# Kernel tuning notes

Hardware: AMD Instinct MI355X
Metric: run time of the kernel (lower is better)

## Reference

```python
import jax, jax.numpy as jnp
import numpy as np

DIM = 256
WINDOW = 8
HEADS = 8
N = WINDOW * WINDOW


def _make_rpb_index(window_size: int) -> jnp.ndarray:
    hs = np.arange(window_size)
    coords = np.stack(np.meshgrid(hs, hs, indexing='ij'))  # [2, w, w]
    flat = coords.reshape(2, -1)                            # [2, N]
    rel = flat[:, :, None] - flat[:, None, :]               # [2, N, N]
    rel = rel.transpose(1, 2, 0).copy()                     # [N, N, 2]
    rel[:, :, 0] += window_size - 1
    rel[:, :, 1] += window_size - 1
    rel[:, :, 0] *= 2 * window_size - 1
    return jnp.asarray(rel.sum(-1), dtype=jnp.int32)        # [N, N]


def setup_inputs() -> dict:
    key = jax.random.key(0)
    k_x, k_qw, k_qb, k_pw, k_pb, k_rpb = jax.random.split(key, 6)
    B_ = 2048
    x = jax.random.normal(k_x, (B_, N, DIM), dtype=jnp.float32)
    mask = jnp.zeros((64, N, N), dtype=jnp.float32)
    # nn.Linear weights stored [out, in] as in torch
    qkv_w = jax.random.normal(k_qw, (3 * DIM, DIM), dtype=jnp.float32) * 0.02
    qkv_b = jnp.zeros((3 * DIM,), dtype=jnp.float32)
    proj_w = jax.random.normal(k_pw, (DIM, DIM), dtype=jnp.float32) * 0.02
    proj_b = jnp.zeros((DIM,), dtype=jnp.float32)
    rpb_table = jax.random.normal(k_rpb, ((2 * WINDOW - 1) ** 2, HEADS), dtype=jnp.float32) * 0.02
    rpb_index = _make_rpb_index(WINDOW)
    return {"x": x, "mask": mask, "qkv_w": qkv_w, "qkv_b": qkv_b,
            "proj_w": proj_w, "proj_b": proj_b, "rpb_table": rpb_table,
            "rpb_index": rpb_index}


def reference(x, mask, qkv_w, qkv_b, proj_w, proj_b, rpb_table, rpb_index):
    B_, n, C = x.shape
    H = HEADS
    d = C // H
    scale = d ** -0.5
    qkv = x @ qkv_w.T + qkv_b                      # [B, N, 3C]
    qkv = qkv.reshape(B_, n, 3, H, d)
    q = qkv[:, :, 0].transpose(0, 2, 1, 3)          # [B, H, N, d]
    k = qkv[:, :, 1].transpose(0, 2, 1, 3)
    v = qkv[:, :, 2].transpose(0, 2, 1, 3)
    attn = jnp.einsum('bhnd,bhmd->bhnm', q * scale, k)
    rpb = rpb_table[rpb_index]                      # [N, N, H]
    attn = attn + rpb.transpose(2, 0, 1)[None]      # [B, H, N, N]
    nW = mask.shape[0]
    attn = attn.reshape(B_ // nW, nW, H, n, n) + mask[None, :, None]
    attn = attn.reshape(B_, H, n, n)
    attn = jax.nn.softmax(attn, axis=-1)
    out = jnp.einsum('bhnm,bhmd->bhnd', attn, v)    # [B, H, N, d]
    out = out.transpose(0, 2, 1, 3).reshape(B_, n, C)
    return out @ proj_w.T + proj_b
```

## Files before the change

kernel.cpp:

```cpp
#include <hip/hip_runtime.h>
#include <hip/hip_bf16.h>


#define TOK 64
#define CDIM 256

typedef __attribute__((ext_vector_type(8))) short short8;
typedef __attribute__((ext_vector_type(4))) float f32x4;
typedef __attribute__((ext_vector_type(4))) float float4_t;

__device__ __forceinline__ short f2bf(float f) {
  union { float f; unsigned u; } v; v.f = f;
  unsigned r = v.u + 0x7FFFu + ((v.u >> 16) & 1u);
  return (short)(r >> 16);
}

__device__ __forceinline__ int rm_addr(int base, int row, int col) {
  return base + row * 512 + ((col * 2) ^ ((row & 7) << 4));
}

__global__ void preconv_kernel(const float* __restrict__ qkv_w,
                               const float* __restrict__ proj_w,
                               const float* __restrict__ rpb_table,
                               const int* __restrict__ rpb_index,
                               short* __restrict__ wqkv,
                               short* __restrict__ wproj,
                               float* __restrict__ rpb_pre) {
  int idx = blockIdx.x * blockDim.x + threadIdx.x;
  const float scale = 0.17677669529663687f;
  if (idx < 768 * 256) {
    float v = qkv_w[idx];
    if (idx < 256 * 256) v *= scale;
    wqkv[idx] = f2bf(v);
  } else if (idx < 768 * 256 + 256 * 256) {
    int i = idx - 768 * 256;
    wproj[i] = f2bf(proj_w[i]);
  } else if (idx < 768 * 256 + 256 * 256 + 8 * 64 * 64) {
    int i = idx - (768 * 256 + 256 * 256);
    int h = i >> 12;
    int nm = i & 4095;
    rpb_pre[i] = rpb_table[rpb_index[nm] * 8 + h];
  }
}

__global__ void __launch_bounds__(512, 2) fused_attn(
    const float* __restrict__ x, const float* __restrict__ mask,
    const float* __restrict__ qkv_b, const float* __restrict__ proj_b,
    const short* __restrict__ wqkv, const short* __restrict__ wproj,
    const float* __restrict__ rpb, float* __restrict__ out) {
  extern __shared__ char smem[];
  const int b = blockIdx.x;
  const int tid = threadIdx.x;
  const int w = tid >> 6;
  const int lane = tid & 63;
  const int lg = lane >> 4;
  const int ll = lane & 15;
  const float scale = 0.17677669529663687f;

  {
    const int row = tid >> 3;
    const int c0 = (tid & 7) * 32;
    const float4_t* src = reinterpret_cast<const float4_t*>(
        x + (size_t)b * TOK * CDIM + row * CDIM + c0);
    for (int j = 0; j < 4; ++j) {
      float4_t f0 = src[2 * j];
      float4_t f1 = src[2 * j + 1];
      short8 s;
      s[0] = f2bf(f0[0]); s[1] = f2bf(f0[1]); s[2] = f2bf(f0[2]); s[3] = f2bf(f0[3]);
      s[4] = f2bf(f1[0]); s[5] = f2bf(f1[1]); s[6] = f2bf(f1[2]); s[7] = f2bf(f1[3]);
      *reinterpret_cast<short8*>(smem + rm_addr(0, row, c0 + 8 * j)) = s;
    }
  }
  __syncthreads();

  f32x4 acc[4][6] = {};
  for (int ks = 0; ks < 8; ++ks) {
    int k0 = ks * 32;
    short8 a[4];
    for (int mi = 0; mi < 4; ++mi)
      a[mi] = *reinterpret_cast<const short8*>(
          smem + rm_addr(0, ll + 16 * mi, k0 + lg * 8));
    for (int j = 0; j < 6; ++j) {
      int s = j >> 1, hf = j & 1;
      int c = s * 256 + w * 32 + hf * 16 + ll;
      short8 bb = *reinterpret_cast<const short8*>(wqkv + c * 256 + k0 + lg * 8);
      for (int mi = 0; mi < 4; ++mi)
        acc[mi][j] = __builtin_amdgcn_mfma_f32_16x16x32_bf16(a[mi], bb, acc[mi][j], 0, 0, 0);
    }
  }
  for (int j = 0; j < 6; ++j) {
    int s = j >> 1, hf = j & 1;
    int c = s * 256 + w * 32 + hf * 16 + ll;
    float bias = qkv_b[c];
    if (s == 0) bias *= scale;
    for (int mi = 0; mi < 4; ++mi) {
      for (int r = 0; r < 4; ++r) {
        int row = lg * 4 + r + 16 * mi;
        short bf = f2bf(acc[mi][j][r] + bias);
        if (s == 0) {
          *reinterpret_cast<short*>(smem + rm_addr(32768, row, w * 32 + hf * 16 + ll)) = bf;
        } else if (s == 1) {
          *reinterpret_cast<short*>(smem + rm_addr(65536, row, w * 32 + hf * 16 + ll)) = bf;
        } else {
          int d = hf * 16 + ll;
          int addr = 98304 + w * 4096 + d * 128 + ((row * 2) ^ ((d & 7) << 4));
          *reinterpret_cast<short*>(smem + addr) = bf;
        }
      }
    }
  }
  __syncthreads();

  f32x4 sa[4][4];
  {
    short8 aq[4], bk[4];
    for (int mi = 0; mi < 4; ++mi)
      aq[mi] = *reinterpret_cast<const short8*>(
          smem + rm_addr(32768, ll + 16 * mi, w * 32 + lg * 8));
    for (int ni = 0; ni < 4; ++ni)
      bk[ni] = *reinterpret_cast<const short8*>(
          smem + rm_addr(65536, ll + 16 * ni, w * 32 + lg * 8));
    f32x4 z{0.0f, 0.0f, 0.0f, 0.0f};
    for (int mi = 0; mi < 4; ++mi)
      for (int ni = 0; ni < 4; ++ni)
        sa[mi][ni] = __builtin_amdgcn_mfma_f32_16x16x32_bf16(aq[mi], bk[ni], z, 0, 0, 0);
    const float* rp = rpb + w * 4096;
    const float* mk = mask + (size_t)(b & 63) * 4096;
    for (int mi = 0; mi < 4; ++mi)
      for (int r = 0; r < 4; ++r) {
        int row = lg * 4 + r + 16 * mi;
        for (int ni = 0; ni < 4; ++ni) {
          int col = ll + 16 * ni;
          sa[mi][ni][r] += rp[row * 64 + col] + mk[row * 64 + col];
        }
      }
  }

  float rinv[4][4];
  for (int mi = 0; mi < 4; ++mi)
    for (int r = 0; r < 4; ++r) {
      float m = sa[mi][0][r];
      for (int ni = 1; ni < 4; ++ni) m = fmaxf(m, sa[mi][ni][r]);
      for (int d = 1; d < 16; d <<= 1) m = fmaxf(m, __shfl_xor(m, d));
      float sum = 0.f;
      for (int ni = 0; ni < 4; ++ni) {
        float e = __expf(sa[mi][ni][r] - m);
        sa[mi][ni][r] = e;
        sum += e;
      }
      for (int d = 1; d < 16; d <<= 1) sum += __shfl_xor(sum, d);
      rinv[mi][r] = 1.0f / sum;
    }

  __syncthreads();

  {
    int base = w * 8192;
    for (int mi = 0; mi < 4; ++mi)
      for (int ni = 0; ni < 4; ++ni)
        for (int r = 0; r < 4; ++r) {
          int row = lg * 4 + r + 16 * mi;
          int col = ll + 16 * ni;
          int addr = base + row * 128 + ((col * 2) ^ ((row & 7) << 4));
          *reinterpret_cast<short*>(smem + addr) = f2bf(sa[mi][ni][r]);
        }
  }
  __syncthreads();

  f32x4 oa[4][2] = {};
  {
    int base = w * 8192;
    for (int ks = 0; ks < 2; ++ks) {
      short8 ap[4];
      for (int mi = 0; mi < 4; ++mi) {
        int row = ll + 16 * mi;
        int addr = base + row * 128 + (((ks * 32 + lg * 8) * 2) ^ ((row & 7) << 4));
        ap[mi] = *reinterpret_cast<const short8*>(smem + addr);
      }
      for (int nj = 0; nj < 2; ++nj) {
        int d = ll + 16 * nj;
        int addr = 98304 + w * 4096 + d * 128 + (((ks * 32 + lg * 8) * 2) ^ ((d & 7) << 4));
        short8 bv = *reinterpret_cast<const short8*>(smem + addr);
        for (int mi = 0; mi < 4; ++mi)
          oa[mi][nj] = __builtin_amdgcn_mfma_f32_16x16x32_bf16(ap[mi], bv, oa[mi][nj], 0, 0, 0);
      }
    }
  }
  for (int mi = 0; mi < 4; ++mi)
    for (int nj = 0; nj < 2; ++nj)
      for (int r = 0; r < 4; ++r) {
        int row = lg * 4 + r + 16 * mi;
        float v = oa[mi][nj][r] * rinv[mi][r];
        *reinterpret_cast<short*>(smem + rm_addr(65536, row, w * 32 + nj * 16 + ll)) = f2bf(v);
      }
  __syncthreads();

  f32x4 pa[4][2] = {};
  for (int ks = 0; ks < 8; ++ks) {
    int k0 = ks * 32;
    short8 a[4];
    for (int mi = 0; mi < 4; ++mi)
      a[mi] = *reinterpret_cast<const short8*>(
          smem + rm_addr(65536, ll + 16 * mi, k0 + lg * 8));
    for (int nj = 0; nj < 2; ++nj) {
      int c = w * 32 + nj * 16 + ll;
      short8 bb = *reinterpret_cast<const short8*>(wproj + c * 256 + k0 + lg * 8);
      for (int mi = 0; mi < 4; ++mi)
        pa[mi][nj] = __builtin_amdgcn_mfma_f32_16x16x32_bf16(a[mi], bb, pa[mi][nj], 0, 0, 0);
    }
  }
  float* outp = out + (size_t)b * TOK * CDIM;
  for (int nj = 0; nj < 2; ++nj) {
    int c = w * 32 + nj * 16 + ll;
    float bias = proj_b[c];
    for (int mi = 0; mi < 4; ++mi)
      for (int r = 0; r < 4; ++r) {
        int row = lg * 4 + r + 16 * mi;
        outp[row * 256 + c] = pa[mi][nj][r] + bias;
      }
  }
}

extern "C" void kernel_launch(void* const* d_in, const int* in_sizes, int n_in,
                              void* d_out, int out_size, void* d_ws, size_t ws_size,
                              hipStream_t stream) {
  const float* x        = (const float*)d_in[0];
  const float* mask     = (const float*)d_in[1];
  const float* qkv_w    = (const float*)d_in[2];
  const float* qkv_b    = (const float*)d_in[3];
  const float* proj_w   = (const float*)d_in[4];
  const float* proj_b   = (const float*)d_in[5];
  const float* rpb_tab  = (const float*)d_in[6];
  const int*   rpb_idx  = (const int*)d_in[7];
  float* out = (float*)d_out;

  short* wqkv = (short*)d_ws;
  short* wproj = wqkv + 768 * 256;
  float* rpb_pre = (float*)(wproj + 256 * 256);

  int total = 768 * 256 + 256 * 256 + 8 * 64 * 64;
  preconv_kernel<<<(total + 255) / 256, 256, 0, stream>>>(
      qkv_w, proj_w, rpb_tab, rpb_idx, wqkv, wproj, rpb_pre);

  hipFuncSetAttribute((const void*)fused_attn,
                      hipFuncAttributeMaxDynamicSharedMemorySize, 131072);
  int B = in_sizes[0] / (TOK * CDIM);
  fused_attn<<<B, 512, 131072, stream>>>(x, mask, qkv_b, proj_b, wqkv, wproj,
                                         rpb_pre, out);
}
```

Before: 243.2 us.

## Halve LDS footprint with per-wave Q/K/V/P buffers and vectorized bias loads

Reworks the shared-memory plan so each wave keeps its Q, K, V and P tiles in its own 8 KB region, with the x tile reusing space. This cuts dynamic LDS from 128 KB to 64 KB, and launch bounds are raised to allow more resident blocks per CU. The relative-position bias and mask are pre-permuted in the prep kernel so each lane reads them as float4. The P tile is written and consumed in two halves without block-wide barriers. The risk is higher register pressure from the 4-blocks launch bound and the extra mask preprocessing pass.

```diff
diff --git a/kernel.cpp b/kernel.cpp
--- a/kernel.cpp
+++ b/kernel.cpp
@@ -4,6 +4,7 @@
 
 #define TOK 64
 #define CDIM 256
+#define XOFF 32768
 
 typedef __attribute__((ext_vector_type(8))) short short8;
 typedef __attribute__((ext_vector_type(4))) float f32x4;
@@ -23,31 +24,51 @@
                                const float* __restrict__ proj_w,
                                const float* __restrict__ rpb_table,
                                const int* __restrict__ rpb_index,
+                               const float* __restrict__ mask,
                                short* __restrict__ wqkv,
                                short* __restrict__ wproj,
-                               float* __restrict__ rpb_pre) {
+                               float* __restrict__ rpbT,
+                               float* __restrict__ maskT) {
   int idx = blockIdx.x * blockDim.x + threadIdx.x;
   const float scale = 0.17677669529663687f;
-  if (idx < 768 * 256) {
+  const int NW1 = 768 * 256;
+  const int NW2 = NW1 + 256 * 256;
+  const int NW3 = NW2 + 8 * 64 * 64;
+  const int NW4 = NW3 + 64 * 64 * 64;
+  if (idx < NW1) {
     float v = qkv_w[idx];
     if (idx < 256 * 256) v *= scale;
     wqkv[idx] = f2bf(v);
-  } else if (idx < 768 * 256 + 256 * 256) {
-    int i = idx - 768 * 256;
+  } else if (idx < NW2) {
+    int i = idx - NW1;
     wproj[i] = f2bf(proj_w[i]);
-  } else if (idx < 768 * 256 + 256 * 256 + 8 * 64 * 64) {
-    int i = idx - (768 * 256 + 256 * 256);
+  } else if (idx < NW3) {
+    int i = idx - NW2;
     int h = i >> 12;
-    int nm = i & 4095;
-    rpb_pre[i] = rpb_table[rpb_index[nm] * 8 + h];
-  }
-}
-
-__global__ void __launch_bounds__(512, 2) fused_attn(
-    const float* __restrict__ x, const float* __restrict__ mask,
-    const float* __restrict__ qkv_b, const float* __restrict__ proj_b,
+    int pos = i & 4095;
+    int qtok = pos >> 6;
+    int t = pos & 63;
+    int llv = t >> 2, ni = t & 3;
+    int kt = ni * 16 + llv;
+    rpbT[i] = rpb_table[rpb_index[qtok * 64 + kt] * 8 + h];
+  } else if (idx < NW4) {
+    int i = idx - NW3;
+    int win = i >> 12;
+    int pos = i & 4095;
+    int qtok = pos >> 6;
+    int t = pos & 63;
+    int llv = t >> 2, ni = t & 3;
+    int kt = ni * 16 + llv;
+    maskT[i] = mask[win * 4096 + qtok * 64 + kt];
+  }
+}
+
+__global__ void __launch_bounds__(512, 4) fused_attn(
+    const float* __restrict__ x, const float* __restrict__ qkv_b,
+    const float* __restrict__ proj_b,
     const short* __restrict__ wqkv, const short* __restrict__ wproj,
-    const float* __restrict__ rpb, float* __restrict__ out) {
+    const float* __restrict__ rpbT, const float* __restrict__ maskT,
+    float* __restrict__ out) {
   extern __shared__ char smem[];
   const int b = blockIdx.x;
   const int tid = threadIdx.x;
@@ -56,6 +77,7 @@
   const int lg = lane >> 4;
   const int ll = lane & 15;
   const float scale = 0.17677669529663687f;
+  const int S0 = w * 8192, S1 = S0 + 4096;
 
   {
     const int row = tid >> 3;
@@ -68,7 +90,7 @@
       short8 s;
       s[0] = f2bf(f0[0]); s[1] = f2bf(f0[1]); s[2] = f2bf(f0[2]); s[3] = f2bf(f0[3]);
       s[4] = f2bf(f1[0]); s[5] = f2bf(f1[1]); s[6] = f2bf(f1[2]); s[7] = f2bf(f1[3]);
-      *reinterpret_cast<short8*>(smem + rm_addr(0, row, c0 + 8 * j)) = s;
+      *reinterpret_cast<short8*>(smem + rm_addr(XOFF, row, c0 + 8 * j)) = s;
     }
   }
   __syncthreads();
@@ -79,7 +101,7 @@
     short8 a[4];
     for (int mi = 0; mi < 4; ++mi)
       a[mi] = *reinterpret_cast<const short8*>(
-          smem + rm_addr(0, ll + 16 * mi, k0 + lg * 8));
+          smem + rm_addr(XOFF, ll + 16 * mi, k0 + lg * 8));
     for (int j = 0; j < 6; ++j) {
       int s = j >> 1, hf = j & 1;
       int c = s * 256 + w * 32 + hf * 16 + ll;
@@ -88,51 +110,58 @@
         acc[mi][j] = __builtin_amdgcn_mfma_f32_16x16x32_bf16(a[mi], bb, acc[mi][j], 0, 0, 0);
     }
   }
-  for (int j = 0; j < 6; ++j) {
+  __syncthreads();
+
+  for (int j = 0; j < 4; ++j) {
     int s = j >> 1, hf = j & 1;
     int c = s * 256 + w * 32 + hf * 16 + ll;
     float bias = qkv_b[c];
     if (s == 0) bias *= scale;
-    for (int mi = 0; mi < 4; ++mi) {
-      for (int r = 0; r < 4; ++r) {
-        int row = lg * 4 + r + 16 * mi;
-        short bf = f2bf(acc[mi][j][r] + bias);
-        if (s == 0) {
-          *reinterpret_cast<short*>(smem + rm_addr(32768, row, w * 32 + hf * 16 + ll)) = bf;
-        } else if (s == 1) {
-          *reinterpret_cast<short*>(smem + rm_addr(65536, row, w * 32 + hf * 16 + ll)) = bf;
-        } else {
-          int d = hf * 16 + ll;
-          int addr = 98304 + w * 4096 + d * 128 + ((row * 2) ^ ((d & 7) << 4));
-          *reinterpret_cast<short*>(smem + addr) = bf;
-        }
-      }
-    }
-  }
-  __syncthreads();
+    int base = (s == 0) ? S0 : S1;
+    int dl2 = (hf * 16 + ll) * 2;
+    for (int mi = 0; mi < 4; ++mi)
+      for (int r = 0; r < 4; ++r) {
+        int tok = lg * 4 + r + 16 * mi;
+        *reinterpret_cast<short*>(smem + base + tok * 64 + (dl2 ^ ((tok & 3) << 4))) =
+            f2bf(acc[mi][j][r] + bias);
+      }
+  }
+  short8 aq[4], bk[4];
+  for (int mi = 0; mi < 4; ++mi)
+    aq[mi] = *reinterpret_cast<const short8*>(
+        smem + S0 + (ll + 16 * mi) * 64 + ((lg * 16) ^ (((ll + 16 * mi) & 3) << 4)));
+  for (int ni = 0; ni < 4; ++ni)
+    bk[ni] = *reinterpret_cast<const short8*>(
+        smem + S1 + (ll + 16 * ni) * 64 + ((lg * 16) ^ (((ll + 16 * ni) & 3) << 4)));
+
+  for (int hf = 0; hf < 2; ++hf) {
+    int c = 2 * 256 + w * 32 + hf * 16 + ll;
+    float bias = qkv_b[c];
+    int d = hf * 16 + ll;
+    for (int mi = 0; mi < 4; ++mi)
+      for (int rp = 0; rp < 2; ++rp) {
+        int tok0 = lg * 4 + rp * 2 + 16 * mi;
+        unsigned u = (unsigned)(unsigned short)f2bf(acc[mi][4 + hf][2 * rp] + bias)
+                   | ((unsigned)(unsigned short)f2bf(acc[mi][4 + hf][2 * rp + 1] + bias) << 16);
+        *reinterpret_cast<unsigned*>(smem + S0 + d * 128 + ((tok0 * 2) ^ ((d & 7) << 4))) = u;
+      }
+  }
 
   f32x4 sa[4][4];
   {
-    short8 aq[4], bk[4];
-    for (int mi = 0; mi < 4; ++mi)
-      aq[mi] = *reinterpret_cast<const short8*>(
-          smem + rm_addr(32768, ll + 16 * mi, w * 32 + lg * 8));
-    for (int ni = 0; ni < 4; ++ni)
-      bk[ni] = *reinterpret_cast<const short8*>(
-          smem + rm_addr(65536, ll + 16 * ni, w * 32 + lg * 8));
     f32x4 z{0.0f, 0.0f, 0.0f, 0.0f};
     for (int mi = 0; mi < 4; ++mi)
       for (int ni = 0; ni < 4; ++ni)
         sa[mi][ni] = __builtin_amdgcn_mfma_f32_16x16x32_bf16(aq[mi], bk[ni], z, 0, 0, 0);
-    const float* rp = rpb + w * 4096;
-    const float* mk = mask + (size_t)(b & 63) * 4096;
-    for (int mi = 0; mi < 4; ++mi)
-      for (int r = 0; r < 4; ++r) {
-        int row = lg * 4 + r + 16 * mi;
-        for (int ni = 0; ni < 4; ++ni) {
-          int col = ll + 16 * ni;
-          sa[mi][ni][r] += rp[row * 64 + col] + mk[row * 64 + col];
-        }
+    const float4_t* rpT4 = reinterpret_cast<const float4_t*>(rpbT) + w * 1024;
+    const float4_t* mkT4 = reinterpret_cast<const float4_t*>(maskT) + (b & 63) * 1024;
+    for (int mi = 0; mi < 4; ++mi)
+      for (int r = 0; r < 4; ++r) {
+        int qtok = lg * 4 + r + 16 * mi;
+        float4_t f = rpT4[qtok * 16 + ll];
+        float4_t g = mkT4[qtok * 16 + ll];
+        for (int ni = 0; ni < 4; ++ni)
+          sa[mi][ni][r] += f[ni] + g[ni];
       }
   }
 
@@ -152,46 +181,40 @@
       rinv[mi][r] = 1.0f / sum;
     }
 
-  __syncthreads();
-
-  {
-    int base = w * 8192;
-    for (int mi = 0; mi < 4; ++mi)
-      for (int ni = 0; ni < 4; ++ni)
+  f32x4 oa[4][2] = {};
+  for (int ks = 0; ks < 2; ++ks) {
+    for (int mi = 0; mi < 4; ++mi)
+      for (int nio = 0; nio < 2; ++nio) {
+        int ni = 2 * ks + nio;
+        int ktl2 = (nio * 16 + ll) * 2;
         for (int r = 0; r < 4; ++r) {
-          int row = lg * 4 + r + 16 * mi;
-          int col = ll + 16 * ni;
-          int addr = base + row * 128 + ((col * 2) ^ ((row & 7) << 4));
-          *reinterpret_cast<short*>(smem + addr) = f2bf(sa[mi][ni][r]);
+          int qtok = lg * 4 + r + 16 * mi;
+          *reinterpret_cast<short*>(smem + S1 + qtok * 64 + (ktl2 ^ ((qtok & 3) << 4))) =
+              f2bf(sa[mi][ni][r]);
         }
-  }
-  __syncthreads();
-
-  f32x4 oa[4][2] = {};
-  {
-    int base = w * 8192;
-    for (int ks = 0; ks < 2; ++ks) {
-      short8 ap[4];
-      for (int mi = 0; mi < 4; ++mi) {
-        int row = ll + 16 * mi;
-        int addr = base + row * 128 + (((ks * 32 + lg * 8) * 2) ^ ((row & 7) << 4));
-        ap[mi] = *reinterpret_cast<const short8*>(smem + addr);
-      }
-      for (int nj = 0; nj < 2; ++nj) {
-        int d = ll + 16 * nj;
-        int addr = 98304 + w * 4096 + d * 128 + (((ks * 32 + lg * 8) * 2) ^ ((d & 7) << 4));
-        short8 bv = *reinterpret_cast<const short8*>(smem + addr);
-        for (int mi = 0; mi < 4; ++mi)
-          oa[mi][nj] = __builtin_amdgcn_mfma_f32_16x16x32_bf16(ap[mi], bv, oa[mi][nj], 0, 0, 0);
-      }
-    }
-  }
+      }
+    short8 ap[4], bv[2];
+    for (int mi = 0; mi < 4; ++mi)
+      ap[mi] = *reinterpret_cast<const short8*>(
+          smem + S1 + (ll + 16 * mi) * 64 + ((lg * 16) ^ (((ll + 16 * mi) & 3) << 4)));
+    for (int njf = 0; njf < 2; ++njf) {
+      int d = njf * 16 + ll;
+      bv[njf] = *reinterpret_cast<const short8*>(
+          smem + S0 + d * 128 + (((ks * 32 + lg * 8) * 2) ^ ((d & 7) << 4)));
+    }
+    for (int mi = 0; mi < 4; ++mi)
+      for (int njf = 0; njf < 2; ++njf)
+        oa[mi][njf] = __builtin_amdgcn_mfma_f32_16x16x32_bf16(ap[mi], bv[njf], oa[mi][njf], 0, 0, 0);
+  }
+
+  __syncthreads();
+
   for (int mi = 0; mi < 4; ++mi)
     for (int nj = 0; nj < 2; ++nj)
       for (int r = 0; r < 4; ++r) {
         int row = lg * 4 + r + 16 * mi;
         float v = oa[mi][nj][r] * rinv[mi][r];
-        *reinterpret_cast<short*>(smem + rm_addr(65536, row, w * 32 + nj * 16 + ll)) = f2bf(v);
+        *reinterpret_cast<short*>(smem + rm_addr(0, row, w * 32 + nj * 16 + ll)) = f2bf(v);
       }
   __syncthreads();
 
@@ -201,7 +224,7 @@
     short8 a[4];
     for (int mi = 0; mi < 4; ++mi)
       a[mi] = *reinterpret_cast<const short8*>(
-          smem + rm_addr(65536, ll + 16 * mi, k0 + lg * 8));
+          smem + rm_addr(0, ll + 16 * mi, k0 + lg * 8));
     for (int nj = 0; nj < 2; ++nj) {
       int c = w * 32 + nj * 16 + ll;
       short8 bb = *reinterpret_cast<const short8*>(wproj + c * 256 + k0 + lg * 8);
@@ -234,17 +257,18 @@
   const int*   rpb_idx  = (const int*)d_in[7];
   float* out = (float*)d_out;
 
-  short* wqkv = (short*)d_ws;
+  short* wqkv  = (short*)d_ws;
   short* wproj = wqkv + 768 * 256;
-  float* rpb_pre = (float*)(wproj + 256 * 256);
-
-  int total = 768 * 256 + 256 * 256 + 8 * 64 * 64;
+  float* rpbT  = (float*)(wproj + 256 * 256);
+  float* maskT = rpbT + 8 * 64 * 64;
+
+  int total = 768 * 256 + 256 * 256 + 8 * 64 * 64 + 64 * 64 * 64;
   preconv_kernel<<<(total + 255) / 256, 256, 0, stream>>>(
-      qkv_w, proj_w, rpb_tab, rpb_idx, wqkv, wproj, rpb_pre);
+      qkv_w, proj_w, rpb_tab, rpb_idx, mask, wqkv, wproj, rpbT, maskT);
 
   hipFuncSetAttribute((const void*)fused_attn,
-                      hipFuncAttributeMaxDynamicSharedMemorySize, 131072);
+                      hipFuncAttributeMaxDynamicSharedMemorySize, 65536);
   int B = in_sizes[0] / (TOK * CDIM);
-  fused_attn<<<B, 512, 131072, stream>>>(x, mask, qkv_b, proj_b, wqkv, wproj,
-                                         rpb_pre, out);
-}
+  fused_attn<<<B, 512, 65536, stream>>>(x, qkv_b, proj_b, wqkv, wproj,
+                                        rpbT, maskT, out);
+}
```

After: 518.3 us. 2.13x slower.
